# Performance work log

Measured on AMD Instinct MI355X. Metric: run time of the kernel, lower is better.

Reference implementation:

```python
import jax, jax.numpy as jnp
import numpy as np

N = 50000
F_IN = 128
HID0, HID1 = 64, 32
HEADS = 2
E = 800000
NEG_SLOPE = 0.2


def gat_conv(x, edge_index, W, att_src, att_dst, bias, heads, out_ch, concat):
    """PyG-style GATConv (add_self_loops=True, negative_slope=0.2, eval mode)."""
    n = x.shape[0]
    loop = jnp.arange(n, dtype=edge_index.dtype)
    src = jnp.concatenate([edge_index[0], loop])  # message sources (x_j)
    dst = jnp.concatenate([edge_index[1], loop])  # message targets (x_i)
    h = (x @ W).reshape(n, heads, out_ch)                # [N,H,C]
    a_src = jnp.einsum('nhc,hc->nh', h, att_src)          # [N,H]
    a_dst = jnp.einsum('nhc,hc->nh', h, att_dst)          # [N,H]
    e = jax.nn.leaky_relu(a_src[src] + a_dst[dst], NEG_SLOPE)  # [E+N,H]
    # segment softmax over incoming edges of each destination node
    m = jax.ops.segment_max(e, dst, num_segments=n)
    m = jnp.where(jnp.isfinite(m), m, 0.0)
    p = jnp.exp(e - m[dst])
    s = jax.ops.segment_sum(p, dst, num_segments=n)
    alpha = p / (s[dst] + 1e-16)                          # [E+N,H]
    msg = h[src] * alpha[:, :, None]                      # [E+N,H,C]
    out = jax.ops.segment_sum(msg, dst, num_segments=n)   # [N,H,C]
    out = out.reshape(n, heads * out_ch) if concat else out.mean(axis=1)
    return out + bias


def setup_inputs() -> dict:
    key = jax.random.key(0)
    ks = jax.random.split(key, 10)
    sc1 = 1.0 / np.sqrt(F_IN)
    sc2 = 1.0 / np.sqrt(HEADS * HID0)
    return {
        'x': jax.random.normal(ks[0], (N, F_IN), dtype=jnp.float32),
        'edge_index': jax.random.randint(ks[1], (2, E), 0, N, dtype=jnp.int64),
        'W1': jax.random.normal(ks[2], (F_IN, HEADS * HID0), dtype=jnp.float32) * sc1,
        'att_src1': jax.random.normal(ks[3], (HEADS, HID0), dtype=jnp.float32) * sc1,
        'att_dst1': jax.random.normal(ks[4], (HEADS, HID0), dtype=jnp.float32) * sc1,
        'bias1': jnp.zeros((HEADS * HID0,), dtype=jnp.float32),
        'W2': jax.random.normal(ks[5], (HEADS * HID0, HEADS * HID1), dtype=jnp.float32) * sc2,
        'att_src2': jax.random.normal(ks[6], (HEADS, HID1), dtype=jnp.float32) * sc2,
        'att_dst2': jax.random.normal(ks[7], (HEADS, HID1), dtype=jnp.float32) * sc2,
        'bias2': jnp.zeros((HID1,), dtype=jnp.float32),
    }


def reference(x, edge_index, W1, att_src1, att_dst1, bias1, W2, att_src2, att_dst2, bias2):
    h = gat_conv(x, edge_index, W1, att_src1, att_dst1, bias1, HEADS, HID0, concat=True)
    h = jax.nn.relu(h)  # Dropout(0.6) is identity in eval mode
    out = gat_conv(h, edge_index, W2, att_src2, att_dst2, bias2, HEADS, HID1, concat=False)
    return out
```

## Files before the change

kernel.cpp:

```cpp
#include <hip/hip_runtime.h>
#include <hip/hip_bf16.h>

#define NN 50000
#define FIN 128
#define NH 2
#define C1 64
#define C2 32
#define NE 800000
#define NEG 0.2f

typedef unsigned int uint32;

__device__ __forceinline__ float lrelu(float v) { return v > 0.0f ? v : NEG * v; }
__device__ __forceinline__ float dot4(float4 a, float4 b) {
    return a.x * b.x + a.y * b.y + a.z * b.z + a.w * b.w;
}
__device__ __forceinline__ uint32 packbf2(float a, float b) {
    uint32 ua = __float_as_uint(a), ub = __float_as_uint(b);
    ua += 0x7fffu + ((ua >> 16) & 1u);
    ub += 0x7fffu + ((ub >> 16) & 1u);
    return (ua >> 16) | (ub & 0xffff0000u);
}
__device__ __forceinline__ void gload16(const float* g, float* l) {
    __builtin_amdgcn_global_load_lds(
        (const __attribute__((address_space(1))) unsigned int*)g,
        (__attribute__((address_space(3))) unsigned int*)l, 16, 0, 0);
}

__global__ void zero_ints(int* __restrict__ a, int n) {
    for (int i = blockIdx.x * blockDim.x + threadIdx.x; i < n;
         i += gridDim.x * blockDim.x) a[i] = 0;
}

__global__ void hist_dst(const int* __restrict__ ei, int* __restrict__ deg) {
    const int i = blockIdx.x * blockDim.x + threadIdx.x;
    if (i >= NE) return;
    atomicAdd(&deg[ei[NE + i]], 1);
}

__global__ void scan_blocks(const int* __restrict__ deg, int* __restrict__ offs,
                            int* __restrict__ bsum) {
    __shared__ int sm[256];
    const int t = threadIdx.x;
    const int i = blockIdx.x * 256 + t;
    const int v = (i < NN) ? deg[i] : 0;
    sm[t] = v;
    __syncthreads();
    int x = v;
    #pragma unroll
    for (int d = 1; d < 256; d <<= 1) {
        const int y = (t >= d) ? sm[t - d] : 0;
        __syncthreads();
        x += y; sm[t] = x;
        __syncthreads();
    }
    if (i < NN) offs[i] = x - v;
    if (t == 255) bsum[blockIdx.x] = x;
}

__global__ void scan_bsums(int* __restrict__ bsum, int nb) {
    __shared__ int sm[256];
    const int t = threadIdx.x;
    const int v = (t < nb) ? bsum[t] : 0;
    sm[t] = v;
    __syncthreads();
    int x = v;
    #pragma unroll
    for (int d = 1; d < 256; d <<= 1) {
        const int y = (t >= d) ? sm[t - d] : 0;
        __syncthreads();
        x += y; sm[t] = x;
        __syncthreads();
    }
    if (t < nb) bsum[t] = x - v;
}

__global__ void scan_add(int* __restrict__ offs, const int* __restrict__ bsum) {
    const int i = blockIdx.x * 256 + threadIdx.x;
    if (i < NN) offs[i] += bsum[blockIdx.x];
}

__global__ void csr_scatter(const int* __restrict__ ei, const int* __restrict__ offs,
                            int* __restrict__ fill, int* __restrict__ esrc) {
    const int i = blockIdx.x * blockDim.x + threadIdx.x;
    if (i >= NE) return;
    const int src = ei[i], dst = ei[NE + i];
    const int pos = offs[dst] + atomicAdd(&fill[dst], 1);
    esrc[pos] = src;
}

template<int BN, bool WRITE_Y, bool WRITE_H16>
__global__ __launch_bounds__(256, 2) void gemm_k128(const float* __restrict__ X,
                                                    const float* __restrict__ Wm,
                                                    const float* __restrict__ attS,
                                                    const float* __restrict__ attD,
                                                    float* __restrict__ Y,
                                                    uint32* __restrict__ H16,
                                                    float* __restrict__ asrcO,
                                                    float* __restrict__ adstO, int M) {
    constexpr int GROUPS = BN / 16;
    constexpr int NR = 256 / GROUPS;
    constexpr int BM = NR * 2;
    constexpr int CS = BN / 4;
    constexpr int NXC = BM / 32;
    constexpr int NWC = BN / 32;
    __shared__ __align__(16) float Xs[2][BM * 32];
    __shared__ __align__(16) float Ws[2][32 * BN];

    const int tid = threadIdx.x;
    const int r  = tid / GROUPS;
    const int g  = tid % GROUPS;
    const int g4 = g * 4;
    const int wv = tid >> 6;
    const int rowBase = blockIdx.x * BM;
    const int rr = r & 7;

    auto stage = [&](int kk, int b) {
        float* XsB = &Xs[b][0];
        float* WsB = &Ws[b][0];
        #pragma unroll
        for (int t = 0; t < NXC; ++t) {
            const int d  = t * 256 + tid;
            const int xr = d >> 3;
            const int kc = (d & 7) ^ (xr & 7);
            int xrow = rowBase + xr;
            if (xrow >= M) xrow = M - 1;
            gload16(X + xrow * 128 + kk * 32 + kc * 4,
                    XsB + (t * 256 + wv * 64) * 4);
        }
        #pragma unroll
        for (int t = 0; t < NWC; ++t) {
            const int d = t * 256 + tid;
            gload16(Wm + kk * 32 * BN + d * 4,
                    WsB + (t * 256 + wv * 64) * 4);
        }
    };

    float4 aA[4], aB[4];
    #pragma unroll
    for (int j = 0; j < 4; ++j) { aA[j] = {0,0,0,0}; aB[j] = {0,0,0,0}; }

    stage(0, 0);
    __syncthreads();
    for (int kk = 0; kk < 4; ++kk) {
        const int cur = kk & 1;
        if (kk < 3) stage(kk + 1, cur ^ 1);
        const float* XsC = &Xs[cur][0];
        const float* WsC = &Ws[cur][0];
        auto step = [&](int k, float xv0, float xv1) {
            const float* wp = WsC + k * BN + g4;
            const float4 w0 = *reinterpret_cast<const float4*>(wp);
            const float4 w1 = *reinterpret_cast<const float4*>(wp + CS);
            const float4 w2 = *reinterpret_cast<const float4*>(wp + 2 * CS);
            const float4 w3 = *reinterpret_cast<const float4*>(wp + 3 * CS);
            aA[0].x += xv0*w0.x; aA[0].y += xv0*w0.y; aA[0].z += xv0*w0.z; aA[0].w += xv0*w0.w;
            aA[1].x += xv0*w1.x; aA[1].y += xv0*w1.y; aA[1].z += xv0*w1.z; aA[1].w += xv0*w1.w;
            aA[2].x += xv0*w2.x; aA[2].y += xv0*w2.y; aA[2].z += xv0*w2.z; aA[2].w += xv0*w2.w;
            aA[3].x += xv0*w3.x; aA[3].y += xv0*w3.y; aA[3].z += xv0*w3.z; aA[3].w += xv0*w3.w;
            aB[0].x += xv1*w0.x; aB[0].y += xv1*w0.y; aB[0].z += xv1*w0.z; aB[0].w += xv1*w0.w;
            aB[1].x += xv1*w1.x; aB[1].y += xv1*w1.y; aB[1].z += xv1*w1.z; aB[1].w += xv1*w1.w;
            aB[2].x += xv1*w2.x; aB[2].y += xv1*w2.y; aB[2].z += xv1*w2.z; aB[2].w += xv1*w2.w;
            aB[3].x += xv1*w3.x; aB[3].y += xv1*w3.y; aB[3].z += xv1*w3.z; aB[3].w += xv1*w3.w;
        };
        #pragma unroll
        for (int kc = 0; kc < 8; ++kc) {
            const float4 xq0 = *reinterpret_cast<const float4*>(
                XsC + (r * 8 + (kc ^ rr)) * 4);
            const float4 xq1 = *reinterpret_cast<const float4*>(
                XsC + ((r + NR) * 8 + (kc ^ rr)) * 4);
            step(kc * 4 + 0, xq0.x, xq1.x);
            step(kc * 4 + 1, xq0.y, xq1.y);
            step(kc * 4 + 2, xq0.z, xq1.z);
            step(kc * 4 + 3, xq0.w, xq1.w);
        }
        __syncthreads();
    }

    const float4* avs = reinterpret_cast<const float4*>(attS);
    const float4* avd = reinterpret_cast<const float4*>(attD);
    #pragma unroll
    for (int p = 0; p < 2; ++p) {
        const float4* a = p ? aB : aA;
        const int grow = rowBase + r + NR * p;
        if (grow < M) {
            if (WRITE_Y) {
                float* yrow = &Y[grow * BN + g4];
                *reinterpret_cast<float4*>(yrow)          = a[0];
                *reinterpret_cast<float4*>(yrow + CS)     = a[1];
                *reinterpret_cast<float4*>(yrow + 2 * CS) = a[2];
                *reinterpret_cast<float4*>(yrow + 3 * CS) = a[3];
            }
            if (WRITE_H16) {
                uint32* hrow = &H16[grow * (BN / 2)];
                #pragma unroll
                for (int j = 0; j < 4; ++j) {
                    uint2 u;
                    u.x = packbf2(a[j].x, a[j].y);
                    u.y = packbf2(a[j].z, a[j].w);
                    *reinterpret_cast<uint2*>(&hrow[g * 2 + j * (CS / 2)]) = u;
                }
            }
        }
        float ps0 = dot4(a[0], avs[g])              + dot4(a[1], avs[g + GROUPS]);
        float ps1 = dot4(a[2], avs[g + 2 * GROUPS]) + dot4(a[3], avs[g + 3 * GROUPS]);
        float pd0 = dot4(a[0], avd[g])              + dot4(a[1], avd[g + GROUPS]);
        float pd1 = dot4(a[2], avd[g + 2 * GROUPS]) + dot4(a[3], avd[g + 3 * GROUPS]);
        #pragma unroll
        for (int d = 1; d < GROUPS; d <<= 1) {
            ps0 += __shfl_xor(ps0, d);
            ps1 += __shfl_xor(ps1, d);
            pd0 += __shfl_xor(pd0, d);
            pd1 += __shfl_xor(pd1, d);
        }
        if (g == 0 && grow < M) {
            asrcO[grow * 2]     = ps0;
            asrcO[grow * 2 + 1] = ps1;
            adstO[grow * 2]     = pd0;
            adstO[grow * 2 + 1] = pd1;
        }
    }
}

__global__ __launch_bounds__(256) void gat_dst1(const int* __restrict__ esrc,
                                                const int* __restrict__ offs,
                                                const uint32* __restrict__ H16,
                                                const float* __restrict__ asrc,
                                                const float* __restrict__ adst,
                                                const float* __restrict__ bias1,
                                                float* __restrict__ out) {
    const int wid  = (blockIdx.x * blockDim.x + threadIdx.x) >> 6;
    const int lane = threadIdx.x & 63;
    if (wid >= NN) return;
    const int dst = wid;
    const int beg = offs[dst];
    const int end = (dst == NN - 1) ? NE : offs[dst + 1];
    const int deg = end - beg;
    const float2 ad = *reinterpret_cast<const float2*>(&adst[dst * 2]);

    int   s0  = 0;
    float pe0 = -INFINITY, pe1 = -INFINITY;
    float m0  = -INFINITY, m1  = -INFINITY;
    for (int j = lane; j < deg; j += 64) {
        const int s = esrc[beg + j];
        const float2 a = *reinterpret_cast<const float2*>(&asrc[s * 2]);
        const float f0 = lrelu(a.x + ad.x);
        const float f1 = lrelu(a.y + ad.y);
        if (j == lane) { s0 = s; pe0 = f0; pe1 = f1; }
        m0 = fmaxf(m0, f0); m1 = fmaxf(m1, f1);
    }
    const float2 aself = *reinterpret_cast<const float2*>(&asrc[dst * 2]);
    const float es0 = lrelu(aself.x + ad.x);
    const float es1 = lrelu(aself.y + ad.y);
    m0 = fmaxf(m0, es0); m1 = fmaxf(m1, es1);
    #pragma unroll
    for (int d = 1; d < 64; d <<= 1) {
        m0 = fmaxf(m0, __shfl_xor(m0, d));
        m1 = fmaxf(m1, __shfl_xor(m1, d));
    }
    const int h = lane >> 5;
    const float m = h ? m1 : m0;

    float l;
    float2 acc;
    {
        const float px = __expf((h ? es1 : es0) - m);
        l = px;
        const uint32 u = H16[dst * 64 + lane];
        acc.x = px * __uint_as_float(u << 16);
        acc.y = px * __uint_as_float(u & 0xffff0000u);
    }
    const int jmax = deg < 64 ? deg : 64;
    int j = 0;
    for (; j + 3 < jmax; j += 4) {
        const int sa = __shfl(s0, j),     sb = __shfl(s0, j + 1);
        const int sc = __shfl(s0, j + 2), sd = __shfl(s0, j + 3);
        const float ta0 = __shfl(pe0, j),     ta1 = __shfl(pe1, j);
        const float tb0 = __shfl(pe0, j + 1), tb1 = __shfl(pe1, j + 1);
        const float tc0 = __shfl(pe0, j + 2), tc1 = __shfl(pe1, j + 2);
        const float td0 = __shfl(pe0, j + 3), td1 = __shfl(pe1, j + 3);
        const uint32 ua = H16[sa * 64 + lane];
        const uint32 ub = H16[sb * 64 + lane];
        const uint32 uc = H16[sc * 64 + lane];
        const uint32 ud = H16[sd * 64 + lane];
        const float pa = __expf((h ? ta1 : ta0) - m);
        const float pb = __expf((h ? tb1 : tb0) - m);
        const float pc = __expf((h ? tc1 : tc0) - m);
        const float pd = __expf((h ? td1 : td0) - m);
        l += (pa + pb) + (pc + pd);
        acc.x += pa * __uint_as_float(ua << 16) + pb * __uint_as_float(ub << 16)
               + pc * __uint_as_float(uc << 16) + pd * __uint_as_float(ud << 16);
        acc.y += pa * __uint_as_float(ua & 0xffff0000u) + pb * __uint_as_float(ub & 0xffff0000u)
               + pc * __uint_as_float(uc & 0xffff0000u) + pd * __uint_as_float(ud & 0xffff0000u);
    }
    for (; j < jmax; ++j) {
        const int s = __shfl(s0, j);
        const float t0 = __shfl(pe0, j), t1 = __shfl(pe1, j);
        const float p = __expf((h ? t1 : t0) - m);
        const uint32 u = H16[s * 64 + lane];
        l += p;
        acc.x += p * __uint_as_float(u << 16);
        acc.y += p * __uint_as_float(u & 0xffff0000u);
    }
    for (int j2 = 64; j2 < deg; ++j2) {
        const int s = esrc[beg + j2];
        const float2 a = *reinterpret_cast<const float2*>(&asrc[s * 2]);
        const float p = __expf(lrelu((h ? a.y : a.x) + (h ? ad.y : ad.x)) - m);
        const uint32 u = H16[s * 64 + lane];
        l += p;
        acc.x += p * __uint_as_float(u << 16);
        acc.y += p * __uint_as_float(u & 0xffff0000u);
    }
    const float inv = 1.0f / (l + 1e-16f);
    const float2 bb = *reinterpret_cast<const float2*>(&bias1[lane * 2]);
    float2 res;
    res.x = fmaxf(acc.x * inv + bb.x, 0.0f);
    res.y = fmaxf(acc.y * inv + bb.y, 0.0f);
    *reinterpret_cast<float2*>(&out[dst * 128 + lane * 2]) = res;
}

__global__ __launch_bounds__(256) void gat_dst2(const int* __restrict__ esrc,
                                                const int* __restrict__ offs,
                                                const float* __restrict__ Hf,
                                                const float* __restrict__ asrc,
                                                const float* __restrict__ adst,
                                                const float* __restrict__ bias,
                                                float* __restrict__ out) {
    const int wid  = (blockIdx.x * blockDim.x + threadIdx.x) >> 6;
    const int lane = threadIdx.x & 63;
    if (wid >= NN) return;
    const int dst = wid;
    const int beg = offs[dst];
    const int end = (dst == NN - 1) ? NE : offs[dst + 1];
    const int deg = end - beg;
    const float2 ad = *reinterpret_cast<const float2*>(&adst[dst * 2]);

    int   s0  = 0;
    float pe0 = -INFINITY, pe1 = -INFINITY;
    float m0  = -INFINITY, m1  = -INFINITY;
    for (int j = lane; j < deg; j += 64) {
        const int s = esrc[beg + j];
        const float2 a = *reinterpret_cast<const float2*>(&asrc[s * 2]);
        const float f0 = lrelu(a.x + ad.x);
        const float f1 = lrelu(a.y + ad.y);
        if (j == lane) { s0 = s; pe0 = f0; pe1 = f1; }
        m0 = fmaxf(m0, f0); m1 = fmaxf(m1, f1);
    }
    const float2 aself = *reinterpret_cast<const float2*>(&asrc[dst * 2]);
    const float es0 = lrelu(aself.x + ad.x);
    const float es1 = lrelu(aself.y + ad.y);
    m0 = fmaxf(m0, es0); m1 = fmaxf(m1, es1);
    #pragma unroll
    for (int d = 1; d < 64; d <<= 1) {
        m0 = fmaxf(m0, __shfl_xor(m0, d));
        m1 = fmaxf(m1, __shfl_xor(m1, d));
    }
    const int h = lane >> 5;
    const float m = h ? m1 : m0;

    float l, acc;
    {
        const float px = __expf((h ? es1 : es0) - m);
        l = px;
        acc = px * Hf[dst * 64 + lane];
    }
    const int jmax = deg < 64 ? deg : 64;
    int j = 0;
    for (; j + 3 < jmax; j += 4) {
        const int sa = __shfl(s0, j),     sb = __shfl(s0, j + 1);
        const int sc = __shfl(s0, j + 2), sd = __shfl(s0, j + 3);
        const float ta0 = __shfl(pe0, j),     ta1 = __shfl(pe1, j);
        const float tb0 = __shfl(pe0, j + 1), tb1 = __shfl(pe1, j + 1);
        const float tc0 = __shfl(pe0, j + 2), tc1 = __shfl(pe1, j + 2);
        const float td0 = __shfl(pe0, j + 3), td1 = __shfl(pe1, j + 3);
        const float ha = Hf[sa * 64 + lane];
        const float hb = Hf[sb * 64 + lane];
        const float hc = Hf[sc * 64 + lane];
        const float hd = Hf[sd * 64 + lane];
        const float pa = __expf((h ? ta1 : ta0) - m);
        const float pb = __expf((h ? tb1 : tb0) - m);
        const float pc = __expf((h ? tc1 : tc0) - m);
        const float pd = __expf((h ? td1 : td0) - m);
        l += (pa + pb) + (pc + pd);
        acc += pa * ha + pb * hb + pc * hc + pd * hd;
    }
    for (; j < jmax; ++j) {
        const int s = __shfl(s0, j);
        const float t0 = __shfl(pe0, j), t1 = __shfl(pe1, j);
        const float p = __expf((h ? t1 : t0) - m);
        const float hv = Hf[s * 64 + lane];
        l += p;
        acc += p * hv;
    }
    for (int j2 = 64; j2 < deg; ++j2) {
        const int s = esrc[beg + j2];
        const float2 a = *reinterpret_cast<const float2*>(&asrc[s * 2]);
        const float p = __expf(lrelu((h ? a.y : a.x) + (h ? ad.y : ad.x)) - m);
        l += p;
        acc += p * Hf[s * 64 + lane];
    }
    float r = acc / (l + 1e-16f);
    r += __shfl_xor(r, 32);
    if (lane < 32) out[dst * 32 + lane] = 0.5f * r + bias[lane];
}

extern "C" void kernel_launch(void* const* d_in, const int* in_sizes, int n_in,
                              void* d_out, int out_size, void* d_ws, size_t ws_size,
                              hipStream_t stream) {
    const float* x   = (const float*)d_in[0];
    const int*   ei  = (const int*)d_in[1];
    const float* W1  = (const float*)d_in[2];
    const float* as1 = (const float*)d_in[3];
    const float* ad1 = (const float*)d_in[4];
    const float* b1  = (const float*)d_in[5];
    const float* W2  = (const float*)d_in[6];
    const float* as2 = (const float*)d_in[7];
    const float* ad2 = (const float*)d_in[8];
    const float* b2  = (const float*)d_in[9];
    float* out = (float*)d_out;

    float* ws = (float*)d_ws;
    size_t off = 0;
    float* out1  = ws + off; off += (size_t)NN * FIN;
    float* h2f   = ws + off; off += (size_t)NN * C1;
    float* asrc1 = ws + off; off += (size_t)NN * NH;
    float* adst1 = ws + off; off += (size_t)NN * NH;
    float* asrc2 = ws + off; off += (size_t)NN * NH;
    float* adst2 = ws + off; off += (size_t)NN * NH;
    uint32* h16  = (uint32*)(ws + off); off += (size_t)NN * 64;
    int* ibase = (int*)(ws + off);
    int* deg   = ibase;
    int* fill  = ibase + NN;
    int* offs  = ibase + 2 * NN;
    int* bsum  = ibase + 3 * NN;
    int* esrc  = ibase + 3 * NN + 256;

    const int B = 256;
    constexpr int NB_SCAN = (NN + 255) / 256;

    zero_ints<<<128, B, 0, stream>>>(deg, 2 * NN);
    hist_dst<<<(NE + B - 1) / B, B, 0, stream>>>(ei, deg);
    scan_blocks<<<NB_SCAN, 256, 0, stream>>>(deg, offs, bsum);
    scan_bsums<<<1, 256, 0, stream>>>(bsum, NB_SCAN);
    scan_add<<<NB_SCAN, 256, 0, stream>>>(offs, bsum);
    csr_scatter<<<(NE + B - 1) / B, B, 0, stream>>>(ei, offs, fill, esrc);

    gemm_k128<128, false, true><<<(NN + 63) / 64, B, 0, stream>>>(
        x, W1, as1, ad1, nullptr, h16, asrc1, adst1, NN);
    gat_dst1<<<(NN * 64 + B - 1) / B, B, 0, stream>>>(
        esrc, offs, h16, asrc1, adst1, b1, out1);

    gemm_k128<64, true, false><<<(NN + 127) / 128, B, 0, stream>>>(
        out1, W2, as2, ad2, h2f, nullptr, asrc2, adst2, NN);
    gat_dst2<<<(NN * 64 + B - 1) / B, B, 0, stream>>>(
        esrc, offs, h2f, asrc2, adst2, b2, out);
}
```

Before: 322.4 us.

## Retile GEMM to 128-thread blocks with 4 rows per thread; store layer-2 features as bf16

```diff
diff --git a/kernel.cpp b/kernel.cpp
--- a/kernel.cpp
+++ b/kernel.cpp
@@ -20,6 +20,9 @@
     ua += 0x7fffu + ((ua >> 16) & 1u);
     ub += 0x7fffu + ((ub >> 16) & 1u);
     return (ua >> 16) | (ub & 0xffff0000u);
+}
+__device__ __forceinline__ float bfsel(uint32 u, int odd) {
+    return __uint_as_float(odd ? (u & 0xffff0000u) : (u << 16));
 }
 __device__ __forceinline__ void gload16(const float* g, float* l) {
     __builtin_amdgcn_global_load_lds(
@@ -89,8 +92,8 @@
     esrc[pos] = src;
 }
 
-template<int BN, bool WRITE_Y, bool WRITE_H16>
-__global__ __launch_bounds__(256, 2) void gemm_k128(const float* __restrict__ X,
+template<int BN, int RPT, bool WRITE_Y, bool WRITE_H16>
+__global__ __launch_bounds__(128, 4) void gemm_k128(const float* __restrict__ X,
                                                     const float* __restrict__ Wm,
                                                     const float* __restrict__ attS,
                                                     const float* __restrict__ attD,
@@ -99,13 +102,14 @@
                                                     float* __restrict__ asrcO,
                                                     float* __restrict__ adstO, int M) {
     constexpr int GROUPS = BN / 16;
-    constexpr int NR = 256 / GROUPS;
-    constexpr int BM = NR * 2;
+    constexpr int NR = 128 / GROUPS;
+    constexpr int BM = NR * RPT;
+    constexpr int KC = 16;
     constexpr int CS = BN / 4;
-    constexpr int NXC = BM / 32;
-    constexpr int NWC = BN / 32;
-    __shared__ __align__(16) float Xs[2][BM * 32];
-    __shared__ __align__(16) float Ws[2][32 * BN];
+    constexpr int NXC = BM * KC / 512;
+    constexpr int NWC = KC * BN / 512;
+    __shared__ __align__(16) float Xs[2][BM * KC];
+    __shared__ __align__(16) float Ws[2][KC * BN];
 
     const int tid = threadIdx.x;
     const int r  = tid / GROUPS;
@@ -113,65 +117,71 @@
     const int g4 = g * 4;
     const int wv = tid >> 6;
     const int rowBase = blockIdx.x * BM;
-    const int rr = r & 7;
+    const int swz = (r >> 1) & 3;
 
     auto stage = [&](int kk, int b) {
         float* XsB = &Xs[b][0];
         float* WsB = &Ws[b][0];
         #pragma unroll
         for (int t = 0; t < NXC; ++t) {
-            const int d  = t * 256 + tid;
-            const int xr = d >> 3;
-            const int kc = (d & 7) ^ (xr & 7);
+            const int d  = t * 128 + tid;
+            const int xr = d >> 2;
+            const int kc = (d & 3) ^ ((xr >> 1) & 3);
             int xrow = rowBase + xr;
             if (xrow >= M) xrow = M - 1;
-            gload16(X + xrow * 128 + kk * 32 + kc * 4,
-                    XsB + (t * 256 + wv * 64) * 4);
+            gload16(X + xrow * 128 + kk * KC + kc * 4,
+                    XsB + (t * 128 + wv * 64) * 4);
         }
         #pragma unroll
         for (int t = 0; t < NWC; ++t) {
-            const int d = t * 256 + tid;
-            gload16(Wm + kk * 32 * BN + d * 4,
-                    WsB + (t * 256 + wv * 64) * 4);
+            const int d = t * 128 + tid;
+            gload16(Wm + kk * KC * BN + d * 4,
+                    WsB + (t * 128 + wv * 64) * 4);
         }
     };
 
-    float4 aA[4], aB[4];
-    #pragma unroll
-    for (int j = 0; j < 4; ++j) { aA[j] = {0,0,0,0}; aB[j] = {0,0,0,0}; }
+    float4 acc[RPT][4];
+    #pragma unroll
+    for (int p = 0; p < RPT; ++p)
+        #pragma unroll
+        for (int j = 0; j < 4; ++j) acc[p][j] = {0, 0, 0, 0};
 
     stage(0, 0);
     __syncthreads();
-    for (int kk = 0; kk < 4; ++kk) {
+    for (int kk = 0; kk < 8; ++kk) {
         const int cur = kk & 1;
-        if (kk < 3) stage(kk + 1, cur ^ 1);
+        if (kk < 7) stage(kk + 1, cur ^ 1);
         const float* XsC = &Xs[cur][0];
         const float* WsC = &Ws[cur][0];
-        auto step = [&](int k, float xv0, float xv1) {
-            const float* wp = WsC + k * BN + g4;
-            const float4 w0 = *reinterpret_cast<const float4*>(wp);
-            const float4 w1 = *reinterpret_cast<const float4*>(wp + CS);
-            const float4 w2 = *reinterpret_cast<const float4*>(wp + 2 * CS);
-            const float4 w3 = *reinterpret_cast<const float4*>(wp + 3 * CS);
-            aA[0].x += xv0*w0.x; aA[0].y += xv0*w0.y; aA[0].z += xv0*w0.z; aA[0].w += xv0*w0.w;
-            aA[1].x += xv0*w1.x; aA[1].y += xv0*w1.y; aA[1].z += xv0*w1.z; aA[1].w += xv0*w1.w;
-            aA[2].x += xv0*w2.x; aA[2].y += xv0*w2.y; aA[2].z += xv0*w2.z; aA[2].w += xv0*w2.w;
-            aA[3].x += xv0*w3.x; aA[3].y += xv0*w3.y; aA[3].z += xv0*w3.z; aA[3].w += xv0*w3.w;
-            aB[0].x += xv1*w0.x; aB[0].y += xv1*w0.y; aB[0].z += xv1*w0.z; aB[0].w += xv1*w0.w;
-            aB[1].x += xv1*w1.x; aB[1].y += xv1*w1.y; aB[1].z += xv1*w1.z; aB[1].w += xv1*w1.w;
-            aB[2].x += xv1*w2.x; aB[2].y += xv1*w2.y; aB[2].z += xv1*w2.z; aB[2].w += xv1*w2.w;
-            aB[3].x += xv1*w3.x; aB[3].y += xv1*w3.y; aB[3].z += xv1*w3.z; aB[3].w += xv1*w3.w;
-        };
         #pragma unroll
-        for (int kc = 0; kc < 8; ++kc) {
-            const float4 xq0 = *reinterpret_cast<const float4*>(
-                XsC + (r * 8 + (kc ^ rr)) * 4);
-            const float4 xq1 = *reinterpret_cast<const float4*>(
-                XsC + ((r + NR) * 8 + (kc ^ rr)) * 4);
-            step(kc * 4 + 0, xq0.x, xq1.x);
-            step(kc * 4 + 1, xq0.y, xq1.y);
-            step(kc * 4 + 2, xq0.z, xq1.z);
-            step(kc * 4 + 3, xq0.w, xq1.w);
+        for (int kc = 0; kc < 4; ++kc) {
+            float4 xq[RPT];
+            #pragma unroll
+            for (int p = 0; p < RPT; ++p)
+                xq[p] = *reinterpret_cast<const float4*>(
+                    XsC + ((r + NR * p) * 4 + (kc ^ swz)) * 4);
+            #pragma unroll
+            for (int e = 0; e < 4; ++e) {
+                const int k = kc * 4 + e;
+                const float* wp = WsC + k * BN + g4;
+                const float4 w0 = *reinterpret_cast<const float4*>(wp);
+                const float4 w1 = *reinterpret_cast<const float4*>(wp + CS);
+                const float4 w2 = *reinterpret_cast<const float4*>(wp + 2 * CS);
+                const float4 w3 = *reinterpret_cast<const float4*>(wp + 3 * CS);
+                #pragma unroll
+                for (int p = 0; p < RPT; ++p) {
+                    const float xv = (e == 0) ? xq[p].x : (e == 1) ? xq[p].y
+                                   : (e == 2) ? xq[p].z : xq[p].w;
+                    acc[p][0].x += xv * w0.x; acc[p][0].y += xv * w0.y;
+                    acc[p][0].z += xv * w0.z; acc[p][0].w += xv * w0.w;
+                    acc[p][1].x += xv * w1.x; acc[p][1].y += xv * w1.y;
+                    acc[p][1].z += xv * w1.z; acc[p][1].w += xv * w1.w;
+                    acc[p][2].x += xv * w2.x; acc[p][2].y += xv * w2.y;
+                    acc[p][2].z += xv * w2.z; acc[p][2].w += xv * w2.w;
+                    acc[p][3].x += xv * w3.x; acc[p][3].y += xv * w3.y;
+                    acc[p][3].z += xv * w3.z; acc[p][3].w += xv * w3.w;
+                }
+            }
         }
         __syncthreads();
     }
@@ -179,8 +189,8 @@
     const float4* avs = reinterpret_cast<const float4*>(attS);
     const float4* avd = reinterpret_cast<const float4*>(attD);
     #pragma unroll
-    for (int p = 0; p < 2; ++p) {
-        const float4* a = p ? aB : aA;
+    for (int p = 0; p < RPT; ++p) {
+        const float4* a = acc[p];
         const int grow = rowBase + r + NR * p;
         if (grow < M) {
             if (WRITE_Y) {
@@ -320,7 +330,7 @@
 
 __global__ __launch_bounds__(256) void gat_dst2(const int* __restrict__ esrc,
                                                 const int* __restrict__ offs,
-                                                const float* __restrict__ Hf,
+                                                const uint32* __restrict__ H16b,
                                                 const float* __restrict__ asrc,
                                                 const float* __restrict__ adst,
                                                 const float* __restrict__ bias,
@@ -332,6 +342,7 @@
     const int beg = offs[dst];
     const int end = (dst == NN - 1) ? NE : offs[dst + 1];
     const int deg = end - beg;
+    const int odd = lane & 1;
     const float2 ad = *reinterpret_cast<const float2*>(&adst[dst * 2]);
 
     int   s0  = 0;
@@ -361,7 +372,7 @@
     {
         const float px = __expf((h ? es1 : es0) - m);
         l = px;
-        acc = px * Hf[dst * 64 + lane];
+        acc = px * bfsel(H16b[dst * 32 + (lane >> 1)], odd);
     }
     const int jmax = deg < 64 ? deg : 64;
     int j = 0;
@@ -372,31 +383,31 @@
         const float tb0 = __shfl(pe0, j + 1), tb1 = __shfl(pe1, j + 1);
         const float tc0 = __shfl(pe0, j + 2), tc1 = __shfl(pe1, j + 2);
         const float td0 = __shfl(pe0, j + 3), td1 = __shfl(pe1, j + 3);
-        const float ha = Hf[sa * 64 + lane];
-        const float hb = Hf[sb * 64 + lane];
-        const float hc = Hf[sc * 64 + lane];
-        const float hd = Hf[sd * 64 + lane];
+        const uint32 ua = H16b[sa * 32 + (lane >> 1)];
+        const uint32 ub = H16b[sb * 32 + (lane >> 1)];
+        const uint32 uc = H16b[sc * 32 + (lane >> 1)];
+        const uint32 ud = H16b[sd * 32 + (lane >> 1)];
         const float pa = __expf((h ? ta1 : ta0) - m);
         const float pb = __expf((h ? tb1 : tb0) - m);
         const float pc = __expf((h ? tc1 : tc0) - m);
         const float pd = __expf((h ? td1 : td0) - m);
         l += (pa + pb) + (pc + pd);
-        acc += pa * ha + pb * hb + pc * hc + pd * hd;
+        acc += pa * bfsel(ua, odd) + pb * bfsel(ub, odd)
+             + pc * bfsel(uc, odd) + pd * bfsel(ud, odd);
     }
     for (; j < jmax; ++j) {
         const int s = __shfl(s0, j);
         const float t0 = __shfl(pe0, j), t1 = __shfl(pe1, j);
         const float p = __expf((h ? t1 : t0) - m);
-        const float hv = Hf[s * 64 + lane];
         l += p;
-        acc += p * hv;
+        acc += p * bfsel(H16b[s * 32 + (lane >> 1)], odd);
     }
     for (int j2 = 64; j2 < deg; ++j2) {
         const int s = esrc[beg + j2];
         const float2 a = *reinterpret_cast<const float2*>(&asrc[s * 2]);
         const float p = __expf(lrelu((h ? a.y : a.x) + (h ? ad.y : ad.x)) - m);
         l += p;
-        acc += p * Hf[s * 64 + lane];
+        acc += p * bfsel(H16b[s * 32 + (lane >> 1)], odd);
     }
     float r = acc / (l + 1e-16f);
     r += __shfl_xor(r, 32);
@@ -421,12 +432,12 @@
     float* ws = (float*)d_ws;
     size_t off = 0;
     float* out1  = ws + off; off += (size_t)NN * FIN;
-    float* h2f   = ws + off; off += (size_t)NN * C1;
     float* asrc1 = ws + off; off += (size_t)NN * NH;
     float* adst1 = ws + off; off += (size_t)NN * NH;
     float* asrc2 = ws + off; off += (size_t)NN * NH;
     float* adst2 = ws + off; off += (size_t)NN * NH;
     uint32* h16  = (uint32*)(ws + off); off += (size_t)NN * 64;
+    uint32* h16b = (uint32*)(ws + off); off += (size_t)NN * 32;
     int* ibase = (int*)(ws + off);
     int* deg   = ibase;
     int* fill  = ibase + NN;
@@ -444,13 +455,13 @@
     scan_add<<<NB_SCAN, 256, 0, stream>>>(offs, bsum);
     csr_scatter<<<(NE + B - 1) / B, B, 0, stream>>>(ei, offs, fill, esrc);
 
-    gemm_k128<128, false, true><<<(NN + 63) / 64, B, 0, stream>>>(
+    gemm_k128<128, 4, false, true><<<(NN + 63) / 64, 128, 0, stream>>>(
         x, W1, as1, ad1, nullptr, h16, asrc1, adst1, NN);
     gat_dst1<<<(NN * 64 + B - 1) / B, B, 0, stream>>>(
         esrc, offs, h16, asrc1, adst1, b1, out1);
 
-    gemm_k128<64, true, false><<<(NN + 127) / 128, B, 0, stream>>>(
-        out1, W2, as2, ad2, h2f, nullptr, asrc2, adst2, NN);
+    gemm_k128<64, 4, false, true><<<(NN + 127) / 128, 128, 0, stream>>>(
+        out1, W2, as2, ad2, nullptr, h16b, asrc2, adst2, NN);
     gat_dst2<<<(NN * 64 + B - 1) / B, B, 0, stream>>>(
-        esrc, offs, h2f, asrc2, adst2, b2, out);
-}
+        esrc, offs, h16b, asrc2, adst2, b2, out);
+}
```

After: 324.9 us. No clear change (+0.8%).
